# Kernel optimization log

Measured on AMD Instinct MI355X. Metric: run time of the kernel, lower is better.

## Reference

```python
import jax, jax.numpy as jnp
import numpy as np

THRESHOLD = 0.5
NEG_POS_RATIO = 3
CONF_WEIGHT = 1.0
VAR = (0.1, 0.1, 0.2, 0.2)
EPS_LOG = 1e-5


def _center_to_corner(p):
    cx, cy, w, h = p[:, 0], p[:, 1], p[:, 2], p[:, 3]
    return jnp.stack([cx - w / 2, cy - h / 2, cx + w / 2, cy + h / 2], axis=1)


def _iou(gt, pr):  # gt [M,4] corners, pr [P,4] corners -> [M,P]
    lt = jnp.maximum(gt[:, None, :2], pr[None, :, :2])
    rb = jnp.minimum(gt[:, None, 2:], pr[None, :, 2:])
    wh = jnp.clip(rb - lt, 0.0)
    inter = wh[..., 0] * wh[..., 1]
    area_g = (gt[:, 2] - gt[:, 0]) * (gt[:, 3] - gt[:, 1])
    area_p = (pr[:, 2] - pr[:, 0]) * (pr[:, 3] - pr[:, 1])
    return inter / (area_g[:, None] + area_p[None, :] - inter + 1e-10)


def _match_one(gt_boxes, priors_corner):
    # standard SSD matching: per-prior best GT if IoU >= threshold, else -1;
    # each GT additionally claims its best prior.
    iou = _iou(gt_boxes, priors_corner)            # [M,P]
    best_gt = jnp.argmax(iou, axis=0)              # [P]
    best_iou = jnp.max(iou, axis=0)                # [P]
    truth = jnp.where(best_iou >= THRESHOLD, best_gt, -1)
    best_prior = jnp.argmax(iou, axis=1)           # [M]
    truth = truth.at[best_prior].set(jnp.arange(gt_boxes.shape[0]))
    return truth


def _encode(matched_gt, priors):
    # matched_gt [B,P,4] corners, priors [P,4] center form -> [B,P,4]
    g_cx = (matched_gt[..., 0] + matched_gt[..., 2]) / 2
    g_cy = (matched_gt[..., 1] + matched_gt[..., 3]) / 2
    g_w = matched_gt[..., 2] - matched_gt[..., 0]
    g_h = matched_gt[..., 3] - matched_gt[..., 1]
    p_cx, p_cy, p_w, p_h = priors[:, 0], priors[:, 1], priors[:, 2], priors[:, 3]
    enc_cx = (g_cx - p_cx) / (p_w * VAR[0])
    enc_cy = (g_cy - p_cy) / (p_h * VAR[1])
    enc_w = jnp.log(g_w / p_w + EPS_LOG) / VAR[2]
    enc_h = jnp.log(g_h / p_h + EPS_LOG) / VAR[3]
    return jnp.stack([enc_cx, enc_cy, enc_w, enc_h], axis=-1)


def setup_inputs() -> dict:
    key = jax.random.key(0)
    ks = jax.random.split(key, 7)
    B, P, C, M = 64, 8732, 81, 20
    pred_loc = jax.random.normal(ks[0], (B, P, 4), jnp.float32)
    pred_conf = jax.random.normal(ks[1], (B, P, C), jnp.float32)
    # priors in center form (cx, cy, w, h)
    p_c = jax.random.uniform(ks[2], (P, 2), jnp.float32)
    p_wh = jax.random.uniform(ks[3], (P, 2), jnp.float32, minval=0.05, maxval=0.5)
    priors = jnp.concatenate([p_c, p_wh], axis=1)
    # GT boxes in corner form, guaranteed valid (x2>x1, y2>y1)
    g_c = jax.random.uniform(ks[4], (B, M, 2), jnp.float32, minval=0.2, maxval=0.8)
    g_wh = jax.random.uniform(ks[5], (B, M, 2), jnp.float32, minval=0.05, maxval=0.3)
    targets_boxes = jnp.concatenate([g_c - g_wh / 2, g_c + g_wh / 2], axis=-1)
    targets_labels = jax.random.randint(ks[6], (B, M), 1, C, jnp.int32)
    return {"pred_loc": pred_loc, "pred_conf": pred_conf, "priors": priors,
            "targets_boxes": targets_boxes, "targets_labels": targets_labels}


def reference(pred_loc, pred_conf, priors, targets_boxes, targets_labels):
    B, P, C = pred_conf.shape
    priors_corner = _center_to_corner(priors)
    truth = jax.vmap(lambda g: _match_one(g, priors_corner))(targets_boxes)  # [B,P]
    pos_mask = truth != -1
    safe = jnp.maximum(truth, 0)
    matched_gt = jax.vmap(lambda t, s: t[s])(targets_boxes, safe)            # [B,P,4]
    target_conf = jnp.where(pos_mask,
                            jax.vmap(lambda l, s: l[s])(targets_labels, safe), 0)

    # localization loss: smooth-L1 (beta=1), sum over matched priors, / batch
    enc = _encode(matched_gt, priors)
    d = pred_loc - enc
    ad = jnp.abs(d)
    sl1 = jnp.where(ad < 1.0, 0.5 * d * d, ad - 0.5)
    loc_loss = jnp.sum(sl1 * pos_mask[..., None]) / B

    # confidence loss with hard negative mining (3:1, double-argsort rank trick)
    logp = jax.nn.log_softmax(pred_conf, axis=-1)                            # [B,P,C]
    ce = -jnp.take_along_axis(logp, target_conf[..., None], axis=-1)[..., 0]  # [B,P]
    ce_neg = jnp.where(pos_mask, 0.0, ce)
    order = jnp.argsort(-ce_neg, axis=1)
    rank = jnp.argsort(order, axis=1)
    pos_num = jnp.sum(pos_mask, axis=1, keepdims=True)
    neg_num = jnp.minimum(NEG_POS_RATIO * pos_num, P - 1)
    neg_mask = rank < neg_num
    prior_mask = pos_mask | neg_mask
    conf_loss = jnp.sum(ce * prior_mask) / jnp.sum(prior_mask) / B * CONF_WEIGHT
    return (loc_loss, conf_loss)
```

## Files before the change

### kernel.cpp

```cpp
#include <hip/hip_runtime.h>
#include <hip/hip_bf16.h>

#define B_   64
#define P_   8732
#define C_   81
#define M_   20
#define BP_  (B_*P_)
#define CEB  64
#define CETH 256
#define NV   (CEB*C_/4)
#define NCH  9
#define SBLK 1024

__global__ __launch_bounds__(256) void iou_kernel(
    const float* __restrict__ priors, const float* __restrict__ tboxes,
    int* __restrict__ truth, unsigned long long* __restrict__ bestc,
    int* __restrict__ pos_cnt, float* __restrict__ pos_sum,
    float* __restrict__ accums, int* __restrict__ done)
{
    const int b = blockIdx.y;
    const int tid = threadIdx.x;

    if (blockIdx.x == 0 && b == 0) {
        if (tid < B_) { pos_cnt[tid] = 0; pos_sum[tid] = 0.f; }
        if (tid >= B_ && tid < B_ + 3) accums[tid - B_] = 0.f;
        if (tid == B_ + 3) *done = 0;
    }

    __shared__ float s_gt[M_][4];
    __shared__ float s_ga[M_];
    __shared__ float s_red[M_][4];
    __shared__ int   s_redp[M_][4];

    if (tid < M_*4) ((float*)s_gt)[tid] = tboxes[b*M_*4 + tid];
    __syncthreads();
    if (tid < M_) s_ga[tid] = (s_gt[tid][2]-s_gt[tid][0]) * (s_gt[tid][3]-s_gt[tid][1]);
    __syncthreads();

    float lb[M_]; int lp[M_];
    #pragma unroll
    for (int m=0;m<M_;++m){ lb[m] = -1.0f; lp[m] = 0x7FFFFFFF; }

    const float4* pr4 = (const float4*)priors;
    const int p0 = blockIdx.x * 1024;
    const int pend = min(p0 + 1024, P_);
    for (int p = p0 + tid; p < pend; p += 256) {
        float4 pc = pr4[p];
        float px0 = pc.x - pc.z*0.5f, py0 = pc.y - pc.w*0.5f;
        float px1 = pc.x + pc.z*0.5f, py1 = pc.y + pc.w*0.5f;
        float pa = pc.z * pc.w;
        float best = -1.0f; int bg = 0;
        #pragma unroll
        for (int m=0;m<M_;++m){
            float ix0 = fmaxf(s_gt[m][0], px0);
            float iy0 = fmaxf(s_gt[m][1], py0);
            float ix1 = fminf(s_gt[m][2], px1);
            float iy1 = fminf(s_gt[m][3], py1);
            float iw = fmaxf(ix1-ix0, 0.f), ih = fmaxf(iy1-iy0, 0.f);
            float inter = iw*ih;
            float iou = inter / (s_ga[m] + pa - inter + 1e-10f);
            if (iou > best) { best = iou; bg = m; }
            if (iou > lb[m]) { lb[m] = iou; lp[m] = p; }
        }
        truth[(size_t)b*P_ + p] = (best >= 0.5f) ? bg : -1;
    }

    const int lane = tid & 63, wid = tid >> 6;
    #pragma unroll
    for (int m=0;m<M_;++m){
        float v = lb[m]; int ip = lp[m];
        for (int off=32; off; off>>=1){
            float ov = __shfl_down(v, off); int op = __shfl_down(ip, off);
            if (ov > v || (ov == v && op < ip)) { v = ov; ip = op; }
        }
        if (lane == 0) { s_red[m][wid] = v; s_redp[m][wid] = ip; }
    }
    __syncthreads();
    if (tid < M_) {
        const int m = tid;
        float v = s_red[m][0]; int ip = s_redp[m][0];
        for (int w=1; w<4; ++w){
            float ov = s_red[m][w]; int op = s_redp[m][w];
            if (ov > v || (ov == v && op < ip)) { v = ov; ip = op; }
        }
        bestc[(b*M_ + m)*NCH + blockIdx.x] =
            ((unsigned long long)__float_as_uint(v) << 32) | (unsigned)(P_ - 1 - ip);
    }
}

__global__ __launch_bounds__(CETH, 7) void ce_loc_kernel(
    const float* __restrict__ pred_conf, const float* __restrict__ pred_loc,
    const float* __restrict__ priors, const float* __restrict__ tboxes,
    const int* __restrict__ tlabels, const int* __restrict__ truth,
    const unsigned long long* __restrict__ bestc,
    float* __restrict__ ce_neg, int* __restrict__ pos_cnt,
    float* __restrict__ pos_sum, float* __restrict__ accums)
{
    __shared__ float sc[CEB * C_];
    __shared__ int   s_fp[2][M_];
    __shared__ int   s_pos[2];
    __shared__ float s_psum[2];
    __shared__ float s_loc[CETH/64];
    const int tid = threadIdx.x;
    const int base = blockIdx.x * CEB;
    const int b0 = base / P_;

    const float4* src4 = (const float4*)(pred_conf + (size_t)base * C_);
    float4* dst4 = (float4*)sc;
#if __has_builtin(__builtin_amdgcn_global_load_lds)
    #pragma unroll
    for (int k = 0; k < NV / CETH; ++k) {
        const int i = tid + k * CETH;
        __builtin_amdgcn_global_load_lds(
            (const __attribute__((address_space(1))) void*)(src4 + i),
            (__attribute__((address_space(3))) void*)(dst4 + i), 16, 0, 0);
    }
    if (tid < NV - (NV / CETH) * CETH) {
        const int i = (NV / CETH) * CETH + tid;
        __builtin_amdgcn_global_load_lds(
            (const __attribute__((address_space(1))) void*)(src4 + i),
            (__attribute__((address_space(3))) void*)(dst4 + i), 16, 0, 0);
    }
#else
    for (int i = tid; i < NV; i += CETH) dst4[i] = src4[i];
#endif

    if (tid < 2*M_) {
        const int j = tid / M_, m = tid - j*M_;
        const int b = b0 + j;
        int p = -1;
        if (b < B_) {
            const unsigned long long* src = &bestc[(b*M_ + m)*NCH];
            unsigned long long best = src[0];
            #pragma unroll
            for (int c = 1; c < NCH; ++c) { unsigned long long kk = src[c]; if (kk > best) best = kk; }
            p = P_ - 1 - (int)(unsigned)(best & 0xFFFFFFFFu);
        }
        s_fp[j][m] = p;
    }
    if (tid < 2) { s_pos[tid] = 0; s_psum[tid] = 0.f; }
    __syncthreads();

    const int r = tid >> 2;
    const int q = tid & 3;
    const float* row = &sc[r * C_];
    const int c0 = q * 20 + (q > 0 ? 1 : 0);
    const int cn = (q == 0) ? 21 : 20;
    float mx = -1e30f;
    for (int c = 0; c < cn; ++c) mx = fmaxf(mx, row[c0 + c]);
    mx = fmaxf(mx, __shfl_xor(mx, 1));
    mx = fmaxf(mx, __shfl_xor(mx, 2));
    float s = 0.f;
    for (int c = 0; c < cn; ++c) s += __expf(row[c0 + c] - mx);
    s += __shfl_xor(s, 1);
    s += __shfl_xor(s, 2);

    float locacc = 0.f;
    if (q == 0) {
        const int bp = base + r;
        const int b = bp / P_;
        const int p = bp - b * P_;
        const int jb = b - b0;
        int t = truth[bp];
        #pragma unroll
        for (int m = 0; m < M_; ++m)
            if (s_fp[jb][m] == p) t = m;
        const int cls = (t >= 0) ? tlabels[b*M_ + t] : 0;
        const float ce = mx + __logf(s) - row[cls];
        if (t >= 0) {
            atomicAdd(&s_pos[jb], 1);
            atomicAdd(&s_psum[jb], ce);
            ce_neg[bp] = 0.f;
            float4 pc = ((const float4*)priors)[p];
            float4 g  = ((const float4*)tboxes)[b*M_ + t];
            float gcx = (g.x+g.z)*0.5f, gcy = (g.y+g.w)*0.5f;
            float gw = g.z - g.x, gh = g.w - g.y;
            float e0 = (gcx - pc.x) / (pc.z * 0.1f);
            float e1 = (gcy - pc.y) / (pc.w * 0.1f);
            float e2 = __logf(gw / pc.z + 1e-5f) * 5.0f;
            float e3 = __logf(gh / pc.w + 1e-5f) * 5.0f;
            float4 pl = ((const float4*)pred_loc)[bp];
            float d0 = pl.x-e0, d1 = pl.y-e1, d2 = pl.z-e2, d3 = pl.w-e3;
            float a0 = fabsf(d0), a1 = fabsf(d1), a2 = fabsf(d2), a3 = fabsf(d3);
            locacc = (a0<1.f ? 0.5f*d0*d0 : a0-0.5f)
                   + (a1<1.f ? 0.5f*d1*d1 : a1-0.5f)
                   + (a2<1.f ? 0.5f*d2*d2 : a2-0.5f)
                   + (a3<1.f ? 0.5f*d3*d3 : a3-0.5f);
        } else {
            ce_neg[bp] = ce;
        }
    }
    for (int off=32; off; off>>=1) locacc += __shfl_down(locacc, off);
    if ((tid & 63) == 0) s_loc[tid>>6] = locacc;
    __syncthreads();
    if (tid == 0) {
        float a = 0.f;
        #pragma unroll
        for (int w = 0; w < CETH/64; ++w) a += s_loc[w];
        if (a != 0.f) atomicAdd(&accums[0], a);
    }
    if (tid < 2) {
        const int br = b0 + tid;
        if (br < B_ && s_pos[tid] > 0) {
            atomicAdd(&pos_cnt[br], s_pos[tid]);
            atomicAdd(&pos_sum[br], s_psum[tid]);
        }
    }
}

__global__ __launch_bounds__(SBLK) void select_kernel(
    const float* __restrict__ ce_neg, const int* __restrict__ pos_cnt,
    const float* __restrict__ pos_sum, float* __restrict__ accums,
    int* __restrict__ done, float* __restrict__ out)
{
    const int b = blockIdx.x; const int tid = threadIdx.x;
    const int lane = tid & 63;
    __shared__ float cl[P_];
    __shared__ unsigned hist[256];
    __shared__ unsigned s_sel, s_prefix, s_remk, s_cntgt;
    __shared__ float s_r1[SBLK/64];
    __shared__ int s_last;

    const float* cerow = ce_neg + (size_t)b * P_;
    if (tid < 256) hist[tid] = 0u;
    if (tid == 0) s_sel = 0u;
    __syncthreads();

    for (int i = tid; i < P_; i += SBLK) {
        const unsigned bin = __float_as_uint(cerow[i]) >> 24;
        unsigned long long todo = __ballot(1);
        while (todo) {
            const int src = (int)__ffsll(todo) - 1;
            const unsigned lead = __shfl(bin, src);
            const unsigned long long mset = __ballot(bin == lead);
            if (lane == src) atomicAdd(&hist[lead], (unsigned)__popcll(mset));
            todo &= ~mset;
        }
    }
    __syncthreads();
    const int pos = pos_cnt[b];
    const unsigned k = (unsigned)min(3 * pos, P_ - 1);
    if (tid == 0) {
        unsigned acc = 0, chosen = 0;
        for (int bin = 255; bin >= 0; --bin) {
            const unsigned c = hist[bin];
            if (acc + c >= k) { chosen = (unsigned)bin; break; }
            acc += c;
        }
        s_prefix = chosen << 24; s_remk = k - acc; s_cntgt = acc;
    }
    __syncthreads();
    const unsigned c3 = s_prefix >> 24;

    float gsum = 0.f;
    for (int i = tid; i < P_; i += SBLK) {
        const float v = cerow[i];
        const unsigned byt = __float_as_uint(v) >> 24;
        if (byt > c3) gsum += v;
        const bool pred = (byt == c3);
        const unsigned long long mset = __ballot(pred);
        if (pred) {
            const int leader = (int)__ffsll(mset) - 1;
            unsigned bse;
            if (lane == leader) bse = atomicAdd(&s_sel, (unsigned)__popcll(mset));
            bse = __shfl(bse, leader);
            cl[bse + __popcll(mset & ((1ull << lane) - 1ull))] = v;
        }
    }
    __syncthreads();
    const int L = (int)s_sel;

    for (int pass = 2; pass >= 0; --pass) {
        if (tid < 256) hist[tid] = 0u;
        __syncthreads();
        const unsigned prefix = s_prefix;
        const int shift = pass * 8;
        const unsigned pmask = 0xFFFFFFFFu << (shift + 8);
        for (int i = tid; i < L; i += SBLK) {
            const unsigned u = __float_as_uint(cl[i]);
            if ((u & pmask) == prefix) atomicAdd(&hist[(u >> shift) & 0xFFu], 1u);
        }
        __syncthreads();
        if (tid == 0) {
            unsigned remk = s_remk, acc = 0, chosen = 0;
            for (int bin = 255; bin >= 0; --bin) {
                const unsigned c = hist[bin];
                if (acc + c >= remk) { chosen = (unsigned)bin; break; }
                acc += c;
            }
            s_cntgt += acc; s_remk = remk - acc; s_prefix = prefix | (chosen << shift);
        }
        __syncthreads();
    }

    const unsigned Tbits = s_prefix;
    const float T = __uint_as_float(Tbits);
    float sgt = gsum;
    for (int i = tid; i < L; i += SBLK) {
        const float v = cl[i];
        if (__float_as_uint(v) > Tbits) sgt += v;
    }
    for (int off=32; off; off>>=1) sgt += __shfl_down(sgt, off);
    if (lane == 0) s_r1[tid>>6] = sgt;
    __syncthreads();
    if (tid == 0) {
        float a = 0.f;
        #pragma unroll
        for (int w = 0; w < SBLK/64; ++w) a += s_r1[w];
        const unsigned sel_eq = s_remk;
        float neg_sum, mc;
        if (Tbits != 0u) { neg_sum = a + (float)sel_eq * T; mc = (float)(pos + (int)k); }
        else             { neg_sum = a;                     mc = (float)(pos + (int)s_cntgt); }
        atomicAdd(&accums[1], pos_sum[b] + neg_sum);
        atomicAdd(&accums[2], mc);
        __threadfence();
        const int old = atomicAdd(done, 1);
        s_last = (old == B_ - 1);
    }
    __syncthreads();
    if (tid == 0 && s_last) {
        const float l  = atomicAdd(&accums[0], 0.f);
        const float cs = atomicAdd(&accums[1], 0.f);
        const float mn = atomicAdd(&accums[2], 0.f);
        out[0] = l / (float)B_;
        out[1] = cs / mn / (float)B_;
    }
}

extern "C" void kernel_launch(void* const* d_in, const int* in_sizes, int n_in,
                              void* d_out, int out_size, void* d_ws, size_t ws_size,
                              hipStream_t stream) {
    (void)in_sizes; (void)n_in; (void)out_size; (void)ws_size;
    const float* pred_loc  = (const float*)d_in[0];
    const float* pred_conf = (const float*)d_in[1];
    const float* priors    = (const float*)d_in[2];
    const float* tboxes    = (const float*)d_in[3];
    const int*   tlabels   = (const int*)d_in[4];
    float* out = (float*)d_out;

    char* ws = (char*)d_ws;
    int*   truth  = (int*)ws;
    float* ce_neg = (float*)(ws + (size_t)BP_ * 4);
    unsigned long long* bestc = (unsigned long long*)(ws + (size_t)BP_ * 8);
    char* tail = ws + (size_t)BP_ * 8 + (size_t)B_*M_*NCH*8;
    int*   pos_cnt = (int*)tail;
    float* pos_sum = (float*)(tail + B_*4);
    float* accums  = (float*)(tail + B_*8);
    int*   done    = (int*)(tail + B_*8 + 12);

    iou_kernel<<<dim3(NCH, B_), 256, 0, stream>>>(priors, tboxes, truth, bestc,
                                                  pos_cnt, pos_sum, accums, done);
    ce_loc_kernel<<<BP_ / CEB, CETH, 0, stream>>>(pred_conf, pred_loc, priors, tboxes,
                                                  tlabels, truth, bestc,
                                                  ce_neg, pos_cnt, pos_sum, accums);
    select_kernel<<<B_, SBLK, 0, stream>>>(ce_neg, pos_cnt, pos_sum, accums, done, out);
}
```

Before: 188.0 us.

## Compute CE per thread from global rows instead of LDS-staged tiles

Drops the LDS staging of pred_conf via global_load_lds and has each thread compute the log-softmax for one prior row directly from global memory, with 4-way split accumulators. Blocks now cover 256 priors instead of 64, and the 4-threads-per-row shuffle reduction is removed. The aim is to cut LDS traffic and synchronization. The cost is strided, poorly coalesced global reads, since each lane reads a separate 324-byte row, and each row is read twice.

```diff
diff --git a/kernel.cpp b/kernel.cpp
--- a/kernel.cpp
+++ b/kernel.cpp
@@ -6,9 +6,6 @@
 #define C_   81
 #define M_   20
 #define BP_  (B_*P_)
-#define CEB  64
-#define CETH 256
-#define NV   (CEB*C_/4)
 #define NCH  9
 #define SBLK 1024
 
@@ -88,7 +85,7 @@
     }
 }
 
-__global__ __launch_bounds__(CETH, 7) void ce_loc_kernel(
+__global__ __launch_bounds__(256) void ce_loc_kernel(
     const float* __restrict__ pred_conf, const float* __restrict__ pred_loc,
     const float* __restrict__ priors, const float* __restrict__ tboxes,
     const int* __restrict__ tlabels, const int* __restrict__ truth,
@@ -96,41 +93,20 @@
     float* __restrict__ ce_neg, int* __restrict__ pos_cnt,
     float* __restrict__ pos_sum, float* __restrict__ accums)
 {
-    __shared__ float sc[CEB * C_];
     __shared__ int   s_fp[2][M_];
     __shared__ int   s_pos[2];
     __shared__ float s_psum[2];
-    __shared__ float s_loc[CETH/64];
+    __shared__ float s_loc[4];
     const int tid = threadIdx.x;
-    const int base = blockIdx.x * CEB;
+    const int base = blockIdx.x * 256;
     const int b0 = base / P_;
-
-    const float4* src4 = (const float4*)(pred_conf + (size_t)base * C_);
-    float4* dst4 = (float4*)sc;
-#if __has_builtin(__builtin_amdgcn_global_load_lds)
-    #pragma unroll
-    for (int k = 0; k < NV / CETH; ++k) {
-        const int i = tid + k * CETH;
-        __builtin_amdgcn_global_load_lds(
-            (const __attribute__((address_space(1))) void*)(src4 + i),
-            (__attribute__((address_space(3))) void*)(dst4 + i), 16, 0, 0);
-    }
-    if (tid < NV - (NV / CETH) * CETH) {
-        const int i = (NV / CETH) * CETH + tid;
-        __builtin_amdgcn_global_load_lds(
-            (const __attribute__((address_space(1))) void*)(src4 + i),
-            (__attribute__((address_space(3))) void*)(dst4 + i), 16, 0, 0);
-    }
-#else
-    for (int i = tid; i < NV; i += CETH) dst4[i] = src4[i];
-#endif
 
     if (tid < 2*M_) {
         const int j = tid / M_, m = tid - j*M_;
-        const int b = b0 + j;
+        const int bb = b0 + j;
         int p = -1;
-        if (b < B_) {
-            const unsigned long long* src = &bestc[(b*M_ + m)*NCH];
+        if (bb < B_) {
+            const unsigned long long* src = &bestc[(bb*M_ + m)*NCH];
             unsigned long long best = src[0];
             #pragma unroll
             for (int c = 1; c < NCH; ++c) { unsigned long long kk = src[c]; if (kk > best) best = kk; }
@@ -141,62 +117,70 @@
     if (tid < 2) { s_pos[tid] = 0; s_psum[tid] = 0.f; }
     __syncthreads();
 
-    const int r = tid >> 2;
-    const int q = tid & 3;
-    const float* row = &sc[r * C_];
-    const int c0 = q * 20 + (q > 0 ? 1 : 0);
-    const int cn = (q == 0) ? 21 : 20;
-    float mx = -1e30f;
-    for (int c = 0; c < cn; ++c) mx = fmaxf(mx, row[c0 + c]);
-    mx = fmaxf(mx, __shfl_xor(mx, 1));
-    mx = fmaxf(mx, __shfl_xor(mx, 2));
-    float s = 0.f;
-    for (int c = 0; c < cn; ++c) s += __expf(row[c0 + c] - mx);
-    s += __shfl_xor(s, 1);
-    s += __shfl_xor(s, 2);
+    const int bp = base + tid;
+    const int b  = bp / P_;
+    const int p  = bp - b * P_;
+    const int jb = b - b0;
+    const float* row = pred_conf + (size_t)bp * C_;
+
+    float m0=-1e30f, m1=-1e30f, m2=-1e30f, m3=-1e30f;
+    #pragma unroll 5
+    for (int c = 0; c < 80; c += 4) {
+        m0 = fmaxf(m0, row[c]);
+        m1 = fmaxf(m1, row[c+1]);
+        m2 = fmaxf(m2, row[c+2]);
+        m3 = fmaxf(m3, row[c+3]);
+    }
+    m0 = fmaxf(m0, row[80]);
+    const float mx = fmaxf(fmaxf(m0, m1), fmaxf(m2, m3));
+
+    float s0=0.f, s1=0.f, s2=0.f, s3=0.f;
+    #pragma unroll 5
+    for (int c = 0; c < 80; c += 4) {
+        s0 += __expf(row[c]   - mx);
+        s1 += __expf(row[c+1] - mx);
+        s2 += __expf(row[c+2] - mx);
+        s3 += __expf(row[c+3] - mx);
+    }
+    s0 += __expf(row[80] - mx);
+    const float s = (s0+s1)+(s2+s3);
+
+    int t = truth[bp];
+    #pragma unroll
+    for (int m = 0; m < M_; ++m)
+        if (s_fp[jb][m] == p) t = m;
+    const int cls = (t >= 0) ? tlabels[b*M_ + t] : 0;
+    const float ce = mx + __logf(s) - row[cls];
 
     float locacc = 0.f;
-    if (q == 0) {
-        const int bp = base + r;
-        const int b = bp / P_;
-        const int p = bp - b * P_;
-        const int jb = b - b0;
-        int t = truth[bp];
-        #pragma unroll
-        for (int m = 0; m < M_; ++m)
-            if (s_fp[jb][m] == p) t = m;
-        const int cls = (t >= 0) ? tlabels[b*M_ + t] : 0;
-        const float ce = mx + __logf(s) - row[cls];
-        if (t >= 0) {
-            atomicAdd(&s_pos[jb], 1);
-            atomicAdd(&s_psum[jb], ce);
-            ce_neg[bp] = 0.f;
-            float4 pc = ((const float4*)priors)[p];
-            float4 g  = ((const float4*)tboxes)[b*M_ + t];
-            float gcx = (g.x+g.z)*0.5f, gcy = (g.y+g.w)*0.5f;
-            float gw = g.z - g.x, gh = g.w - g.y;
-            float e0 = (gcx - pc.x) / (pc.z * 0.1f);
-            float e1 = (gcy - pc.y) / (pc.w * 0.1f);
-            float e2 = __logf(gw / pc.z + 1e-5f) * 5.0f;
-            float e3 = __logf(gh / pc.w + 1e-5f) * 5.0f;
-            float4 pl = ((const float4*)pred_loc)[bp];
-            float d0 = pl.x-e0, d1 = pl.y-e1, d2 = pl.z-e2, d3 = pl.w-e3;
-            float a0 = fabsf(d0), a1 = fabsf(d1), a2 = fabsf(d2), a3 = fabsf(d3);
-            locacc = (a0<1.f ? 0.5f*d0*d0 : a0-0.5f)
-                   + (a1<1.f ? 0.5f*d1*d1 : a1-0.5f)
-                   + (a2<1.f ? 0.5f*d2*d2 : a2-0.5f)
-                   + (a3<1.f ? 0.5f*d3*d3 : a3-0.5f);
-        } else {
-            ce_neg[bp] = ce;
-        }
-    }
+    if (t >= 0) {
+        atomicAdd(&s_pos[jb], 1);
+        atomicAdd(&s_psum[jb], ce);
+        ce_neg[bp] = 0.f;
+        float4 pc = ((const float4*)priors)[p];
+        float4 g  = ((const float4*)tboxes)[b*M_ + t];
+        float gcx = (g.x+g.z)*0.5f, gcy = (g.y+g.w)*0.5f;
+        float gw = g.z - g.x, gh = g.w - g.y;
+        float e0 = (gcx - pc.x) / (pc.z * 0.1f);
+        float e1 = (gcy - pc.y) / (pc.w * 0.1f);
+        float e2 = __logf(gw / pc.z + 1e-5f) * 5.0f;
+        float e3 = __logf(gh / pc.w + 1e-5f) * 5.0f;
+        float4 pl = ((const float4*)pred_loc)[bp];
+        float d0 = pl.x-e0, d1 = pl.y-e1, d2 = pl.z-e2, d3 = pl.w-e3;
+        float a0 = fabsf(d0), a1 = fabsf(d1), a2 = fabsf(d2), a3 = fabsf(d3);
+        locacc = (a0<1.f ? 0.5f*d0*d0 : a0-0.5f)
+               + (a1<1.f ? 0.5f*d1*d1 : a1-0.5f)
+               + (a2<1.f ? 0.5f*d2*d2 : a2-0.5f)
+               + (a3<1.f ? 0.5f*d3*d3 : a3-0.5f);
+    } else {
+        ce_neg[bp] = ce;
+    }
+
     for (int off=32; off; off>>=1) locacc += __shfl_down(locacc, off);
     if ((tid & 63) == 0) s_loc[tid>>6] = locacc;
     __syncthreads();
     if (tid == 0) {
-        float a = 0.f;
-        #pragma unroll
-        for (int w = 0; w < CETH/64; ++w) a += s_loc[w];
+        float a = s_loc[0]+s_loc[1]+s_loc[2]+s_loc[3];
         if (a != 0.f) atomicAdd(&accums[0], a);
     }
     if (tid < 2) {
@@ -350,8 +334,8 @@
 
     iou_kernel<<<dim3(NCH, B_), 256, 0, stream>>>(priors, tboxes, truth, bestc,
                                                   pos_cnt, pos_sum, accums, done);
-    ce_loc_kernel<<<BP_ / CEB, CETH, 0, stream>>>(pred_conf, pred_loc, priors, tboxes,
-                                                  tlabels, truth, bestc,
-                                                  ce_neg, pos_cnt, pos_sum, accums);
+    ce_loc_kernel<<<BP_ / 256, 256, 0, stream>>>(pred_conf, pred_loc, priors, tboxes,
+                                                 tlabels, truth, bestc,
+                                                 ce_neg, pos_cnt, pos_sum, accums);
     select_kernel<<<B_, SBLK, 0, stream>>>(ce_neg, pos_cnt, pos_sum, accums, done, out);
 }
```

Measured after the change: 176.0 us. -6.4%, faster.
